# Performance work log

Measured on AMD Instinct MI355X. Metric: run time of the kernel, lower is better.

## Reference

```python
import jax, jax.numpy as jnp
import numpy as np

B, S, D = 2, 2048, 2048
H, G = 16, 4
DH = D // H  # 128
KV = G * DH  # 512


def setup_inputs() -> dict:
    key = jax.random.key(0)
    ks = jax.random.split(key, 10)
    scale = 1.0 / np.sqrt(D)
    hidden_state = jax.random.normal(ks[0], (B, S, D), dtype=jnp.float32)
    # causal mask: 1 above the diagonal (positions to block), 0 elsewhere
    casual_mask = jnp.triu(jnp.ones((S, S), dtype=jnp.float32), k=1)
    padding_mask = jnp.zeros((B, S), dtype=jnp.float32)
    Wq = jax.random.normal(ks[1], (D, D), dtype=jnp.float32) * scale
    bq = jnp.zeros((D,), dtype=jnp.float32)
    Wk = jax.random.normal(ks[2], (D, KV), dtype=jnp.float32) * scale
    bk = jnp.zeros((KV,), dtype=jnp.float32)
    Wv = jax.random.normal(ks[3], (D, KV), dtype=jnp.float32) * scale
    bv = jnp.zeros((KV,), dtype=jnp.float32)
    Wo = jax.random.normal(ks[4], (D, D), dtype=jnp.float32) * scale
    bo = jnp.zeros((D,), dtype=jnp.float32)
    return {"hidden_state": hidden_state, "casual_mask": casual_mask,
            "padding_mask": padding_mask, "Wq": Wq, "bq": bq, "Wk": Wk,
            "bk": bk, "Wv": Wv, "bv": bv, "Wo": Wo, "bo": bo}


def reference(hidden_state, casual_mask, padding_mask, Wq, bq, Wk, bk, Wv, bv, Wo, bo):
    b, s, _ = hidden_state.shape
    rep = H // G  # heads per KV group
    q = (hidden_state @ Wq + bq).reshape(b, s, H, DH).transpose(0, 2, 1, 3)  # [b,H,s,dh]
    k = (hidden_state @ Wk + bk).reshape(b, s, G, DH).transpose(0, 2, 1, 3)  # [b,G,s,dh]
    v = (hidden_state @ Wv + bv).reshape(b, s, G, DH).transpose(0, 2, 1, 3)
    # expand KV heads: each group serves H//G query heads
    k = jnp.repeat(k, rep, axis=1)  # [b,H,s,dh]
    v = jnp.repeat(v, rep, axis=1)
    scores = jnp.einsum('bhqd,bhkd->bhqk', q, k) / jnp.sqrt(jnp.float32(DH))
    scores = scores + casual_mask * (-1e9)
    scores = scores + padding_mask[:, None, None, :] * (-1e9)
    attn = jax.nn.softmax(scores, axis=-1)
    out = jnp.einsum('bhqk,bhkd->bhqd', attn, v)  # [b,H,s,dh]
    out = out.transpose(0, 2, 1, 3).reshape(b, s, D)
    return out @ Wo + bo
```

## Files before the change

kernel.cpp:

```cpp
#include <hip/hip_runtime.h>
#include <math.h>

typedef unsigned short u16;
typedef __bf16 bf16_t;
typedef u16 u16x4 __attribute__((ext_vector_type(4)));
typedef u16 u16x8 __attribute__((ext_vector_type(8)));
typedef bf16_t bf16x8 __attribute__((ext_vector_type(8)));
typedef float f32x4 __attribute__((ext_vector_type(4)));

__device__ __forceinline__ float bf2f(u16 v) {
    union { unsigned u; float f; } x; x.u = ((unsigned)v) << 16; return x.f;
}
__device__ __forceinline__ u16 f2bf(float f) {
    union { float f; unsigned u; } x; x.f = f;
    unsigned u = x.u;
    return (u16)((u + 0x7fffu + ((u >> 16) & 1u)) >> 16);
}

__device__ __forceinline__ void gload16(const u16* g, u16* l) {
    __builtin_amdgcn_global_load_lds(
        (const __attribute__((address_space(1))) void*)g,
        (__attribute__((address_space(3))) void*)l,
        16, 0, 0);
}

__device__ __forceinline__ bool is_bf16_input(const unsigned* __restrict__ probe) {
    unsigned w = probe[(threadIdx.x & 63) * 32771 + 7];
    unsigned b7 = (w >> 8) & 0x7f;
    bool hit = (b7 >= 0x38) && (b7 <= 0x3f);
    return __builtin_popcountll(__ballot(hit)) >= 32;
}

__global__ __launch_bounds__(256) void convert_kernel(
    const void* __restrict__ src, u16* __restrict__ dst, int n,
    const unsigned* __restrict__ probe)
{
    bool bf = is_bf16_input(probe);
    int i = (blockIdx.x * 256 + threadIdx.x) * 8;
    if (i >= n) return;
    if (bf) {
        *(u16x8*)&dst[i] = *(const u16x8*)&((const u16*)src)[i];
    } else {
        const float* s = (const float*)src + i;
        u16x8 o;
#pragma unroll
        for (int j = 0; j < 8; j++) o[j] = f2bf(s[j]);
        *(u16x8*)&dst[i] = o;
    }
}

__global__ __launch_bounds__(256) void tconv_kernel(
    const void* __restrict__ in, u16* __restrict__ out, int R, int C,
    const unsigned* __restrict__ probe)
{
    bool bf = is_bf16_input(probe);
    __shared__ u16 t[32][33];
    int x = threadIdx.x & 31, y = threadIdx.x >> 5;
    int bx = blockIdx.x * 32, by = blockIdx.y * 32;
    if (bf) {
        const u16* s = (const u16*)in;
#pragma unroll
        for (int i = 0; i < 32; i += 8)
            t[y + i][x] = s[(size_t)(by + y + i) * C + bx + x];
    } else {
        const float* s = (const float*)in;
#pragma unroll
        for (int i = 0; i < 32; i += 8)
            t[y + i][x] = f2bf(s[(size_t)(by + y + i) * C + bx + x]);
    }
    __syncthreads();
#pragma unroll
    for (int i = 0; i < 32; i += 8)
        out[(size_t)(bx + y + i) * R + by + x] = t[x][y + i];
}

__global__ __launch_bounds__(256) void transpose_kernel(
    const u16* __restrict__ in, u16* __restrict__ out, int R, int LD)
{
    __shared__ u16 t[32][33];
    int x = threadIdx.x & 31, y = threadIdx.x >> 5;
    int bx = blockIdx.x * 32, by = blockIdx.y * 32;
#pragma unroll
    for (int i = 0; i < 32; i += 8)
        t[y + i][x] = in[(size_t)(by + y + i) * LD + bx + x];
    __syncthreads();
#pragma unroll
    for (int i = 0; i < 32; i += 8)
        out[(size_t)(bx + y + i) * R + by + x] = t[x][y + i];
}

__global__ __launch_bounds__(256) void gemm_bias_kernel(
    const u16* __restrict__ A, const u16* __restrict__ BT,
    const u16* __restrict__ bias, void* __restrict__ Cout,
    int M, int N, int K, const unsigned* __restrict__ probe, float scale)
{
    __shared__ __align__(16) u16 As[128 * 32];
    __shared__ __align__(16) u16 Bs[128 * 32];
    const int tid  = threadIdx.x;
    const int lane = tid & 63, wave = tid >> 6;
    const int quad = lane >> 4, li = lane & 15;
    const int bm = blockIdx.x * 128, bn = blockIdx.y * 128;
    const int wm = (wave >> 1) * 64, wn = (wave & 1) * 64;
    const int lrow = lane >> 2;
    const int lcol = (lane & 3) * 8;

    f32x4 acc[4][4] = {};

    for (int k0 = 0; k0 < K; k0 += 32) {
#pragma unroll
        for (int j = 0; j < 2; j++) {
            int c = wave * 2 + j;
            int row = c * 16 + lrow;
            gload16(&A [(size_t)(bm + row) * K + k0 + lcol], &As[c * 16 * 32]);
            gload16(&BT[(size_t)(bn + row) * K + k0 + lcol], &Bs[c * 16 * 32]);
        }
        __syncthreads();
        bf16x8 af[4], bfr[4];
#pragma unroll
        for (int i = 0; i < 4; i++)
            af[i]  = *(const bf16x8*)&As[(wm + i * 16 + li) * 32 + quad * 8];
#pragma unroll
        for (int i = 0; i < 4; i++)
            bfr[i] = *(const bf16x8*)&Bs[(wn + i * 16 + li) * 32 + quad * 8];
#pragma unroll
        for (int mt = 0; mt < 4; mt++)
#pragma unroll
            for (int nt = 0; nt < 4; nt++)
                acc[mt][nt] = __builtin_amdgcn_mfma_f32_16x16x32_bf16(
                    af[mt], bfr[nt], acc[mt][nt], 0, 0, 0);
        __syncthreads();
    }

    bool bf = probe ? is_bf16_input(probe) : true;
    if (bf) {
        u16* C16 = (u16*)Cout;
#pragma unroll
        for (int nt = 0; nt < 4; nt++) {
            int col = bn + wn + nt * 16 + li;
            float bb = bf2f(bias[col]);
#pragma unroll
            for (int mt = 0; mt < 4; mt++)
#pragma unroll
                for (int r = 0; r < 4; r++) {
                    int row = bm + wm + mt * 16 + quad * 4 + r;
                    C16[(size_t)row * N + col] = f2bf((acc[mt][nt][r] + bb) * scale);
                }
        }
    } else {
        float* Cf = (float*)Cout;
#pragma unroll
        for (int nt = 0; nt < 4; nt++) {
            int col = bn + wn + nt * 16 + li;
            float bb = bf2f(bias[col]);
#pragma unroll
            for (int mt = 0; mt < 4; mt++)
#pragma unroll
                for (int r = 0; r < 4; r++) {
                    int row = bm + wm + mt * 16 + quad * 4 + r;
                    Cf[(size_t)row * N + col] = (acc[mt][nt][r] + bb) * scale;
                }
        }
    }
}

__global__ __launch_bounds__(256) void flash_kernel(
    const u16* __restrict__ Q, const u16* __restrict__ Kg,
    const u16* __restrict__ VT, u16* __restrict__ O)
{
    constexpr int S = 2048, D = 2048, DH = 128, QKSTR = 3072;
    constexpr float SCALE = 0.08838834764831845f;
    __shared__ __align__(16) u16 Ks[32 * 136];
    __shared__ __align__(16) u16 Vt[128 * 40];
    __shared__ __align__(16) u16 Pw[4][32 * 40];

    const int tid  = threadIdx.x;
    const int wave = tid >> 6, lane = tid & 63;
    const int quad = lane >> 4, li = lane & 15;
    const int qt = blockIdx.x, h = blockIdx.y, b = blockIdx.z;
    const int g = h >> 2;
    const int q0w = qt * 128 + wave * 32;

    const u16* Qb = Q  + (size_t)b * S * QKSTR;
    const u16* Kb = Kg + (size_t)b * S * QKSTR;
    const u16* Vg = VT + (size_t)g * DH * (2 * S) + (size_t)b * S;

    bf16x8 qf[2][4];
#pragma unroll
    for (int m = 0; m < 2; m++)
#pragma unroll
        for (int c = 0; c < 4; c++)
            qf[m][c] = *(const bf16x8*)&Qb[(size_t)(q0w + m * 16 + li) * QKSTR
                                           + h * DH + c * 32 + quad * 8];

    f32x4 oacc[2][8] = {};
    float mr[2] = { -INFINITY, -INFINITY };
    float lr[2] = { 0.f, 0.f };

    const int kend = qt * 128 + 128;

    u16x8 kreg[2], vreg[2];
#pragma unroll
    for (int ch = 0; ch < 2; ch++) {
        int idx = tid + ch * 256;
        kreg[ch] = *(const u16x8*)&Kb[(size_t)(idx >> 4) * QKSTR + g * DH + (idx & 15) * 8];
        vreg[ch] = *(const u16x8*)&Vg[(size_t)(idx >> 2) * (2 * S) + (idx & 3) * 8];
    }

    for (int kc = 0; kc < kend; kc += 32) {
#pragma unroll
        for (int ch = 0; ch < 2; ch++) {
            int idx = tid + ch * 256;
            *(u16x8*)&Ks[(idx >> 4) * 136 + (idx & 15) * 8] = kreg[ch];
            *(u16x8*)&Vt[(idx >> 2) * 40  + (idx & 3) * 8]  = vreg[ch];
        }
        __syncthreads();

        int kn = kc + 32;
        if (kn < kend) {
#pragma unroll
            for (int ch = 0; ch < 2; ch++) {
                int idx = tid + ch * 256;
                kreg[ch] = *(const u16x8*)&Kb[(size_t)(kn + (idx >> 4)) * QKSTR
                                              + g * DH + (idx & 15) * 8];
                vreg[ch] = *(const u16x8*)&Vg[(size_t)(idx >> 2) * (2 * S)
                                              + kn + (idx & 3) * 8];
            }
        }

        if (kc <= q0w) {
            f32x4 sacc[2][2] = {};
#pragma unroll
            for (int t = 0; t < 2; t++)
#pragma unroll
                for (int c = 0; c < 4; c++) {
                    bf16x8 kf = *(const bf16x8*)&Ks[(t * 16 + li) * 136 + c * 32 + quad * 8];
#pragma unroll
                    for (int m = 0; m < 2; m++)
                        sacc[m][t] = __builtin_amdgcn_mfma_f32_16x16x32_bf16(
                            kf, qf[m][c], sacc[m][t], 0, 0, 0);
                }

            float alpha_b[2][4];
#pragma unroll
            for (int m = 0; m < 2; m++) {
                int row = q0w + m * 16 + li;
                f32x4 s0 = sacc[m][0] * SCALE;
                f32x4 s1 = sacc[m][1] * SCALE;
#pragma unroll
                for (int r = 0; r < 4; r++) {
                    int k0 = kc + quad * 4 + r;
                    if (k0 > row)      s0[r] = -INFINITY;
                    if (k0 + 16 > row) s1[r] = -INFINITY;
                }
                float mx = fmaxf(fmaxf(fmaxf(s0[0], s0[1]), fmaxf(s0[2], s0[3])),
                                 fmaxf(fmaxf(s1[0], s1[1]), fmaxf(s1[2], s1[3])));
                mx = fmaxf(mx, __shfl_xor(mx, 16));
                mx = fmaxf(mx, __shfl_xor(mx, 32));
                float mnew = fmaxf(mr[m], mx);
                float al = __expf(mr[m] - mnew);
                mr[m] = mnew;
                f32x4 p0, p1;
                float ps = 0.f;
#pragma unroll
                for (int r = 0; r < 4; r++) {
                    p0[r] = __expf(s0[r] - mnew);
                    p1[r] = __expf(s1[r] - mnew);
                    ps += p0[r] + p1[r];
                }
                ps += __shfl_xor(ps, 16);
                ps += __shfl_xor(ps, 32);
                lr[m] = lr[m] * al + ps;
                u16x4 c0, c1;
#pragma unroll
                for (int r = 0; r < 4; r++) { c0[r] = f2bf(p0[r]); c1[r] = f2bf(p1[r]); }
                *(u16x4*)&Pw[wave][(m * 16 + li) * 40 + quad * 4]      = c0;
                *(u16x4*)&Pw[wave][(m * 16 + li) * 40 + 16 + quad * 4] = c1;
#pragma unroll
                for (int r = 0; r < 4; r++)
                    alpha_b[m][r] = __shfl(al, quad * 4 + r, 16);
            }

#pragma unroll
            for (int m = 0; m < 2; m++)
#pragma unroll
                for (int dt = 0; dt < 8; dt++)
#pragma unroll
                    for (int r = 0; r < 4; r++)
                        oacc[m][dt][r] *= alpha_b[m][r];

            asm volatile("s_waitcnt lgkmcnt(0)" ::: "memory");
            union { u16x8 u; bf16x8 bv; } pc0, pc1;
            pc0.u = *(const u16x8*)&Pw[wave][(0 * 16 + li) * 40 + quad * 8];
            pc1.u = *(const u16x8*)&Pw[wave][(1 * 16 + li) * 40 + quad * 8];
            bf16x8 pf[2] = { pc0.bv, pc1.bv };

#pragma unroll
            for (int dt = 0; dt < 8; dt++) {
                bf16x8 vf = *(const bf16x8*)&Vt[(dt * 16 + li) * 40 + quad * 8];
#pragma unroll
                for (int m = 0; m < 2; m++)
                    oacc[m][dt] = __builtin_amdgcn_mfma_f32_16x16x32_bf16(
                        pf[m], vf, oacc[m][dt], 0, 0, 0);
            }
        }
        __syncthreads();
    }

    u16* Ob = O + (size_t)b * S * D;
#pragma unroll
    for (int m = 0; m < 2; m++) {
#pragma unroll
        for (int r = 0; r < 4; r++) {
            float linv = 1.0f / __shfl(lr[m], quad * 4 + r, 16);
            int row = q0w + m * 16 + quad * 4 + r;
#pragma unroll
            for (int dt = 0; dt < 8; dt++)
                Ob[(size_t)row * D + h * DH + dt * 16 + li] = f2bf(oacc[m][dt][r] * linv);
        }
    }
}

extern "C" void kernel_launch(void* const* d_in, const int* in_sizes, int n_in,
                              void* d_out, int out_size, void* d_ws, size_t ws_size,
                              hipStream_t stream)
{
    const void* X  = d_in[0];
    const void* Wq = d_in[3];
    const void* bq = d_in[4];
    const void* Wk = d_in[5];
    const void* bk = d_in[6];
    const void* Wv = d_in[7];
    const void* bv = d_in[8];
    const void* Wo = d_in[9];
    const void* bo = d_in[10];
    const unsigned* probe = (const unsigned*)d_in[3];

    u16* ws    = (u16*)d_ws;
    u16* Xc    = ws;
    u16* WqkvT = Xc    + 8388608;
    u16* bqkv  = WqkvT + 6291456;
    u16* boc   = bqkv  + 3072;
    u16* QKV   = boc   + 2048;
    u16* VTb   = QKV   + 12582912;
    u16* Ob    = VTb   + 2097152;

    convert_kernel<<<4096, 256, 0, stream>>>(X,  Xc,  8388608, probe);
    convert_kernel<<<1,    256, 0, stream>>>(bq, bqkv,        2048, probe);
    convert_kernel<<<1,    256, 0, stream>>>(bk, bqkv + 2048, 512,  probe);
    convert_kernel<<<1,    256, 0, stream>>>(bv, bqkv + 2560, 512,  probe);
    convert_kernel<<<1,    256, 0, stream>>>(bo, boc, 2048, probe);

    tconv_kernel<<<dim3(64, 64), 256, 0, stream>>>(Wq, WqkvT,                  2048, 2048, probe);
    tconv_kernel<<<dim3(16, 64), 256, 0, stream>>>(Wk, WqkvT + 2048 * 2048,    2048, 512,  probe);
    tconv_kernel<<<dim3(16, 64), 256, 0, stream>>>(Wv, WqkvT + 2560 * 2048,    2048, 512,  probe);

    gemm_bias_kernel<<<dim3(32, 24), 256, 0, stream>>>(Xc, WqkvT, bqkv, QKV,
                                                       4096, 3072, 2048, nullptr, 1.0f);

    transpose_kernel<<<dim3(16, 128), 256, 0, stream>>>(QKV + 2560, VTb, 4096, 3072);

    flash_kernel<<<dim3(16, 16, 2), 256, 0, stream>>>(QKV, QKV + 2048, VTb, Ob);

    tconv_kernel<<<dim3(64, 64), 256, 0, stream>>>(Wo, WqkvT, 2048, 2048, probe);

    gemm_bias_kernel<<<dim3(32, 16), 256, 0, stream>>>(Ob, WqkvT, boc, d_out,
                                                       4096, 2048, 2048, probe, 1.0f);
}
```

Baseline: 460.5 us.

## Split long causal query tiles across two blocks and merge partial softmax results

```diff
diff --git a/kernel.cpp b/kernel.cpp
--- a/kernel.cpp
+++ b/kernel.cpp
@@ -91,8 +91,10 @@
 
 __global__ __launch_bounds__(256) void gemm_bias_kernel(
     const u16* __restrict__ A, const u16* __restrict__ BT,
-    const u16* __restrict__ bias, void* __restrict__ Cout,
-    int M, int N, int K, const unsigned* __restrict__ probe, float scale)
+    const void* __restrict__ bias0, const void* __restrict__ bias1,
+    const void* __restrict__ bias2, void* __restrict__ Cout,
+    int M, int N, int K, const unsigned* __restrict__ probe,
+    int out_native, float scale)
 {
     __shared__ __align__(16) u16 As[128 * 32];
     __shared__ __align__(16) u16 Bs[128 * 32];
@@ -131,13 +133,18 @@
         __syncthreads();
     }
 
-    bool bf = probe ? is_bf16_input(probe) : true;
-    if (bf) {
-        u16* C16 = (u16*)Cout;
-#pragma unroll
-        for (int nt = 0; nt < 4; nt++) {
-            int col = bn + wn + nt * 16 + li;
-            float bb = bf2f(bias[col]);
+    const bool bf_in = is_bf16_input(probe);
+    const bool out_bf = out_native ? bf_in : true;
+#pragma unroll
+    for (int nt = 0; nt < 4; nt++) {
+        int col = bn + wn + nt * 16 + li;
+        const void* bp; int bc;
+        if (col < 2048)      { bp = bias0; bc = col; }
+        else if (col < 2560) { bp = bias1; bc = col - 2048; }
+        else                 { bp = bias2; bc = col - 2560; }
+        float bb = bf_in ? bf2f(((const u16*)bp)[bc]) : ((const float*)bp)[bc];
+        if (out_bf) {
+            u16* C16 = (u16*)Cout;
 #pragma unroll
             for (int mt = 0; mt < 4; mt++)
 #pragma unroll
@@ -145,13 +152,8 @@
                     int row = bm + wm + mt * 16 + quad * 4 + r;
                     C16[(size_t)row * N + col] = f2bf((acc[mt][nt][r] + bb) * scale);
                 }
-        }
-    } else {
-        float* Cf = (float*)Cout;
-#pragma unroll
-        for (int nt = 0; nt < 4; nt++) {
-            int col = bn + wn + nt * 16 + li;
-            float bb = bf2f(bias[col]);
+        } else {
+            float* Cf = (float*)Cout;
 #pragma unroll
             for (int mt = 0; mt < 4; mt++)
 #pragma unroll
@@ -163,9 +165,10 @@
     }
 }
 
-__global__ __launch_bounds__(256) void flash_kernel(
+__global__ __launch_bounds__(256, 4) void flash_kernel(
     const u16* __restrict__ Q, const u16* __restrict__ Kg,
-    const u16* __restrict__ VT, u16* __restrict__ O)
+    const u16* __restrict__ VT, u16* __restrict__ O,
+    float* __restrict__ PO, float* __restrict__ PM, float* __restrict__ PL)
 {
     constexpr int S = 2048, D = 2048, DH = 128, QKSTR = 3072;
     constexpr float SCALE = 0.08838834764831845f;
@@ -176,7 +179,14 @@
     const int tid  = threadIdx.x;
     const int wave = tid >> 6, lane = tid & 63;
     const int quad = lane >> 4, li = lane & 15;
-    const int qt = blockIdx.x, h = blockIdx.y, b = blockIdx.z;
+    const int uu = blockIdx.x, h = blockIdx.y, b = blockIdx.z;
+    const int split = (uu >= 10) ? 1 : 0;
+    const int qt = split ? (10 + ((uu - 10) >> 1)) : uu;
+    const int cc = split ? ((uu - 10) & 1) : 0;
+    const int tiles = qt + 1;
+    const int kmid = (tiles >> 1) * 128;
+    const int kstart = cc ? kmid : 0;
+    const int kend = (split && !cc) ? kmid : tiles * 128;
     const int g = h >> 2;
     const int q0w = qt * 128 + wave * 32;
 
@@ -196,17 +206,17 @@
     float mr[2] = { -INFINITY, -INFINITY };
     float lr[2] = { 0.f, 0.f };
 
-    const int kend = qt * 128 + 128;
-
     u16x8 kreg[2], vreg[2];
 #pragma unroll
     for (int ch = 0; ch < 2; ch++) {
         int idx = tid + ch * 256;
-        kreg[ch] = *(const u16x8*)&Kb[(size_t)(idx >> 4) * QKSTR + g * DH + (idx & 15) * 8];
-        vreg[ch] = *(const u16x8*)&Vg[(size_t)(idx >> 2) * (2 * S) + (idx & 3) * 8];
-    }
-
-    for (int kc = 0; kc < kend; kc += 32) {
+        kreg[ch] = *(const u16x8*)&Kb[(size_t)(kstart + (idx >> 4)) * QKSTR
+                                      + g * DH + (idx & 15) * 8];
+        vreg[ch] = *(const u16x8*)&Vg[(size_t)(idx >> 2) * (2 * S)
+                                      + kstart + (idx & 3) * 8];
+    }
+
+    for (int kc = kstart; kc < kend; kc += 32) {
 #pragma unroll
         for (int ch = 0; ch < 2; ch++) {
             int idx = tid + ch * 256;
@@ -306,17 +316,70 @@
         __syncthreads();
     }
 
-    u16* Ob = O + (size_t)b * S * D;
-#pragma unroll
-    for (int m = 0; m < 2; m++) {
-#pragma unroll
-        for (int r = 0; r < 4; r++) {
-            float linv = 1.0f / __shfl(lr[m], quad * 4 + r, 16);
-            int row = q0w + m * 16 + quad * 4 + r;
-#pragma unroll
-            for (int dt = 0; dt < 8; dt++)
-                Ob[(size_t)row * D + h * DH + dt * 16 + li] = f2bf(oacc[m][dt][r] * linv);
-        }
+    if (!split) {
+        u16* Ob = O + (size_t)b * S * D;
+#pragma unroll
+        for (int m = 0; m < 2; m++) {
+#pragma unroll
+            for (int r = 0; r < 4; r++) {
+                float linv = 1.0f / __shfl(lr[m], quad * 4 + r, 16);
+                int row = q0w + m * 16 + quad * 4 + r;
+#pragma unroll
+                for (int dt = 0; dt < 8; dt++)
+                    Ob[(size_t)row * D + h * DH + dt * 16 + li] =
+                        f2bf(oacc[m][dt][r] * linv);
+            }
+        }
+    } else {
+        const int gu = (b * 16 + h) * 12 + (qt - 10) * 2 + cc;
+        float* POu = PO + (size_t)gu * 16384;
+#pragma unroll
+        for (int m = 0; m < 2; m++)
+#pragma unroll
+            for (int r = 0; r < 4; r++) {
+                int rl = wave * 32 + m * 16 + quad * 4 + r;
+#pragma unroll
+                for (int dt = 0; dt < 8; dt++)
+                    POu[rl * 128 + dt * 16 + li] = oacc[m][dt][r];
+            }
+        if (quad == 0) {
+#pragma unroll
+            for (int m = 0; m < 2; m++) {
+                int rl = wave * 32 + m * 16 + li;
+                PM[gu * 128 + rl] = mr[m];
+                PL[gu * 128 + rl] = lr[m];
+            }
+        }
+    }
+}
+
+__global__ __launch_bounds__(256) void combine_kernel(
+    const float* __restrict__ PO, const float* __restrict__ PM,
+    const float* __restrict__ PL, u16* __restrict__ O)
+{
+    constexpr int S = 2048, D = 2048;
+    const int qt = 10 + blockIdx.x, h = blockIdx.y, b = blockIdx.z;
+    const int g0 = (b * 16 + h) * 12 + blockIdx.x * 2;
+    const int t = threadIdx.x;
+    const int row = t >> 1, half = (t & 1) * 64;
+
+    float m0 = PM[g0 * 128 + row], m1 = PM[(g0 + 1) * 128 + row];
+    float l0 = PL[g0 * 128 + row], l1 = PL[(g0 + 1) * 128 + row];
+    float M = fmaxf(m0, m1);
+    float w0 = __expf(m0 - M), w1 = __expf(m1 - M);
+    float linv = 1.0f / (l0 * w0 + l1 * w1);
+
+    const float* p0 = PO + (size_t)g0 * 16384 + row * 128 + half;
+    const float* p1 = p0 + 16384;
+    u16* out = O + (size_t)(b * S + qt * 128 + row) * D + h * 128 + half;
+#pragma unroll
+    for (int j = 0; j < 64; j += 4) {
+        f32x4 a = *(const f32x4*)&p0[j];
+        f32x4 c = *(const f32x4*)&p1[j];
+        u16x4 o;
+#pragma unroll
+        for (int e = 0; e < 4; e++) o[e] = f2bf((a[e] * w0 + c[e] * w1) * linv);
+        *(u16x4*)&out[j] = o;
     }
 }
 
@@ -338,31 +401,31 @@
     u16* ws    = (u16*)d_ws;
     u16* Xc    = ws;
     u16* WqkvT = Xc    + 8388608;
-    u16* bqkv  = WqkvT + 6291456;
-    u16* boc   = bqkv  + 3072;
-    u16* QKV   = boc   + 2048;
+    u16* QKV   = WqkvT + 6291456;
     u16* VTb   = QKV   + 12582912;
     u16* Ob    = VTb   + 2097152;
-
-    convert_kernel<<<4096, 256, 0, stream>>>(X,  Xc,  8388608, probe);
-    convert_kernel<<<1,    256, 0, stream>>>(bq, bqkv,        2048, probe);
-    convert_kernel<<<1,    256, 0, stream>>>(bk, bqkv + 2048, 512,  probe);
-    convert_kernel<<<1,    256, 0, stream>>>(bv, bqkv + 2560, 512,  probe);
-    convert_kernel<<<1,    256, 0, stream>>>(bo, boc, 2048, probe);
-
-    tconv_kernel<<<dim3(64, 64), 256, 0, stream>>>(Wq, WqkvT,                  2048, 2048, probe);
-    tconv_kernel<<<dim3(16, 64), 256, 0, stream>>>(Wk, WqkvT + 2048 * 2048,    2048, 512,  probe);
-    tconv_kernel<<<dim3(16, 64), 256, 0, stream>>>(Wv, WqkvT + 2560 * 2048,    2048, 512,  probe);
-
-    gemm_bias_kernel<<<dim3(32, 24), 256, 0, stream>>>(Xc, WqkvT, bqkv, QKV,
-                                                       4096, 3072, 2048, nullptr, 1.0f);
+    float* PO  = (float*)ws;
+    float* PM  = PO + 384 * 16384;
+    float* PL  = PM + 384 * 128;
+
+    convert_kernel<<<4096, 256, 0, stream>>>(X, Xc, 8388608, probe);
+
+    tconv_kernel<<<dim3(64, 64), 256, 0, stream>>>(Wq, WqkvT,               2048, 2048, probe);
+    tconv_kernel<<<dim3(16, 64), 256, 0, stream>>>(Wk, WqkvT + 2048 * 2048, 2048, 512,  probe);
+    tconv_kernel<<<dim3(16, 64), 256, 0, stream>>>(Wv, WqkvT + 2560 * 2048, 2048, 512,  probe);
+
+    gemm_bias_kernel<<<dim3(32, 24), 256, 0, stream>>>(
+        Xc, WqkvT, bq, bk, bv, QKV, 4096, 3072, 2048, probe, 0, 1.0f);
 
     transpose_kernel<<<dim3(16, 128), 256, 0, stream>>>(QKV + 2560, VTb, 4096, 3072);
 
-    flash_kernel<<<dim3(16, 16, 2), 256, 0, stream>>>(QKV, QKV + 2048, VTb, Ob);
+    flash_kernel<<<dim3(22, 16, 2), 256, 0, stream>>>(
+        QKV, QKV + 2048, VTb, Ob, PO, PM, PL);
+
+    combine_kernel<<<dim3(6, 16, 2), 256, 0, stream>>>(PO, PM, PL, Ob);
 
     tconv_kernel<<<dim3(64, 64), 256, 0, stream>>>(Wo, WqkvT, 2048, 2048, probe);
 
-    gemm_bias_kernel<<<dim3(32, 16), 256, 0, stream>>>(Ob, WqkvT, boc, d_out,
-                                                       4096, 2048, 2048, probe, 1.0f);
-}
+    gemm_bias_kernel<<<dim3(32, 16), 256, 0, stream>>>(
+        Ob, WqkvT, bo, bo, bo, d_out, 4096, 2048, 2048, probe, 1, 1.0f);
+}
```

Result: slower. 584.2 us (+26.9%).
